# Kernel optimization log

Measured on AMD Instinct MI355X. Metric: run time of the kernel, lower is better.

The kernel has to match this reference:

```python
import jax, jax.numpy as jnp
import numpy as np

B, N, OBS, ACT, H = 262144, 3, 30, 5, 64
IN = OBS + ACT  # 35
NEG_SLOPE_ATT = 0.2   # PyG GATConv default
NEG_SLOPE_MLP = 0.01
LN_EPS = 1e-5


def setup_inputs() -> dict:
    key = jax.random.key(0)
    ks = jax.random.split(key, 24)
    p = lambda k, shape, s=0.1: jax.random.normal(k, shape, jnp.float32) * s
    return {
        "obs": jax.random.normal(ks[0], (B, N * OBS), jnp.float32),
        "action": jax.random.normal(ks[1], (B, N * ACT), jnp.float32),
        "adj_matrix": jax.random.randint(ks[2], (B, N, N), 0, 2, jnp.int32),
        # GAT layer 1 (in=35 -> out=64, 1 head)
        "W1": p(ks[3], (IN, H)), "a1s": p(ks[4], (H,)), "a1d": p(ks[5], (H,)), "b1": jnp.zeros((H,), jnp.float32),
        # GAT layer 2 (in=64 -> out=64, 1 head)
        "W2": p(ks[6], (H, H)), "a2s": p(ks[7], (H,)), "a2d": p(ks[8], (H,)), "b2": jnp.zeros((H,), jnp.float32),
        # output_net: Linear(192,256)+LN, Linear(256,128)+LN, Linear(128,1)
        "Wo1": p(ks[9], (N * H, 256)), "bo1": jnp.zeros((256,), jnp.float32),
        "g1": jnp.ones((256,), jnp.float32), "be1": jnp.zeros((256,), jnp.float32),
        "Wo2": p(ks[10], (256, 128)), "bo2": jnp.zeros((128,), jnp.float32),
        "g2": jnp.ones((128,), jnp.float32), "be2": jnp.zeros((128,), jnp.float32),
        "Wo3": p(ks[11], (128, 1)), "bo3": jnp.zeros((1,), jnp.float32),
    }


def _gat(x, W, a_s, a_d, b, count):
    # x: [B,N,Din], count[b,i,j] = multiplicity of edge j->i (adj^T + self loop)
    z = jnp.einsum('bnd,de->bne', x, W)                      # [B,N,H]
    s_src = jnp.einsum('bnd,d->bn', z, a_s)                  # score contrib of source j
    s_dst = jnp.einsum('bnd,d->bn', z, a_d)                  # score contrib of target i
    e = jax.nn.leaky_relu(s_src[:, None, :] + s_dst[:, :, None], NEG_SLOPE_ATT)  # e[b,i,j]
    cnt = count.astype(z.dtype)
    m = jnp.max(jnp.where(count > 0, e, -jnp.inf), axis=-1, keepdims=True)  # self-loop guarantees finite
    p = cnt * jnp.exp(e - m)                                 # multiplicity-weighted softmax numerator
    alpha = p / jnp.sum(p, axis=-1, keepdims=True)           # [B,N,N]
    return jnp.einsum('bij,bjd->bid', alpha, z) + b


def _ln(x, g, be):
    mu = jnp.mean(x, axis=-1, keepdims=True)
    v = jnp.mean(jnp.square(x - mu), axis=-1, keepdims=True)
    return (x - mu) * jax.lax.rsqrt(v + LN_EPS) * g + be


def reference(obs, action, adj_matrix, W1, a1s, a1d, b1, W2, a2s, a2d, b2,
              Wo1, bo1, g1, be1, Wo2, bo2, g2, be2, Wo3, bo3):
    Bsz = obs.shape[0]
    x = jnp.concatenate([obs.reshape(Bsz, N, OBS), action.reshape(Bsz, N, ACT)], axis=-1)  # [B,N,35]
    # edge multiplicity: adj[b,s,t] means edge s->t; plus one self-loop per node
    count = jnp.swapaxes(adj_matrix, 1, 2) + jnp.eye(N, dtype=adj_matrix.dtype)  # count[b,i,j]
    h = jax.nn.elu(_gat(x, W1, a1s, a1d, b1, count))
    h = _gat(h, W2, a2s, a2d, b2, count)
    h = h.reshape(Bsz, N * H)
    h = jax.nn.leaky_relu(_ln(h @ Wo1 + bo1, g1, be1), NEG_SLOPE_MLP)
    h = jax.nn.leaky_relu(_ln(h @ Wo2 + bo2, g2, be2), NEG_SLOPE_MLP)
    return h @ Wo3 + bo3  # [B,1]
```

## Files before the change

kernel.cpp:

```cpp
#include <hip/hip_runtime.h>
#include <hip/hip_bf16.h>
#include <stdint.h>

#define B_TOT 262144

typedef __attribute__((ext_vector_type(8))) short bf8;
typedef __attribute__((ext_vector_type(16))) float f32x16;

__device__ __forceinline__ uint32_t f2bf(float x) {
  uint32_t u = __float_as_uint(x);
  return (u + 0x7fffu + ((u >> 16) & 1u)) >> 16;
}
__device__ __forceinline__ uint32_t pkbf(float lo, float hi) {
  union { __hip_bfloat162 b; uint32_t u; } c;
  c.b = __float22bfloat162_rn(make_float2(lo, hi));
  return c.u;
}
__device__ __forceinline__ bf8 mkfrag(uint32_t w0, uint32_t w1, uint32_t w2, uint32_t w3) {
  union { uint32_t u[4]; bf8 v; } c;
  c.u[0] = w0; c.u[1] = w1; c.u[2] = w2; c.u[3] = w3;
  return c.v;
}
__device__ __forceinline__ bf8 u4bf8(uint4 v) {
  union { uint4 u; bf8 b; } c; c.u = v; return c.b;
}
__device__ __forceinline__ int swz(int c, int q) { return c * 16 + (q ^ (c & 15)); }

__global__ __launch_bounds__(256) void prep_kernel(
    const int* __restrict__ adj,
    const float* __restrict__ W1, const float* __restrict__ a1s, const float* __restrict__ a1d,
    const float* __restrict__ W2, const float* __restrict__ a2s, const float* __restrict__ a2d,
    const float* __restrict__ Wo1, const float* __restrict__ Wo2,
    uint32_t* __restrict__ cntp, uint16_t* __restrict__ W1F, uint16_t* __restrict__ W2F,
    uint16_t* __restrict__ Wo1F, uint16_t* __restrict__ Wo2F, float* __restrict__ wvec)
{
  const int gid = blockIdx.x * 256 + threadIdx.x;
  if (gid < B_TOT) {
    uint32_t cpv = 0;
    const int* ap = adj + (size_t)gid * 9;
    #pragma unroll
    for (int i = 0; i < 3; ++i)
      #pragma unroll
      for (int j = 0; j < 3; ++j) {
        uint32_t c = (uint32_t)ap[j * 3 + i] + (i == j ? 1u : 0u);
        cpv |= c << (2 * (3 * i + j));
      }
    cntp[gid] = cpv;
  }
  const int e = gid & 7, li = (gid >> 3) & 63;
  const int kfrag = 8 * (e >> 2) + 4 * (li >> 5) + (e & 3);
  if (gid < 3072) {
    const int f = gid >> 9, t = f & 1, ks = f >> 1;
    const int k = ks * 16 + kfrag, row = t * 32 + (li & 31);
    W1F[gid] = (uint16_t)f2bf(k < 35 ? W1[k * 64 + row] : 0.f);
  }
  if (gid < 4096) {
    const int f = gid >> 9, t = f & 1, ks = f >> 1;
    const int k = ks * 16 + kfrag, row = t * 32 + (li & 31);
    W2F[gid] = (uint16_t)f2bf(W2[k * 64 + row]);
  }
  if (gid < 49152) {
    const int rr = gid >> 9, t = rr & 7, ks = rr >> 3;
    const int k = ks * 16 + kfrag, col = t * 32 + (li & 31);
    Wo1F[gid] = (uint16_t)f2bf(Wo1[k * 256 + col]);
  }
  if (gid < 32768) {
    const int rr = gid >> 9, t = rr & 3, ks = rr >> 2;
    const int k = ks * 16 + kfrag, col = t * 32 + (li & 31);
    Wo2F[gid] = (uint16_t)f2bf(Wo2[k * 128 + col]);
  }
  if (gid < 224) {
    if (gid < 48) {
      float s = 0.f; if (gid < 35) for (int d = 0; d < 64; ++d) s += W1[gid * 64 + d] * a1s[d];
      wvec[gid] = s;
    } else if (gid < 96) {
      const int k = gid - 48; float s = 0.f;
      if (k < 35) for (int d = 0; d < 64; ++d) s += W1[k * 64 + d] * a1d[d];
      wvec[64 + k] = s;
    } else if (gid < 160) {
      const int k = gid - 96; float s = 0.f;
      for (int d = 0; d < 64; ++d) s += W2[k * 64 + d] * a2s[d];
      wvec[128 + k] = s;
    } else {
      const int k = gid - 160; float s = 0.f;
      for (int d = 0; d < 64; ++d) s += W2[k * 64 + d] * a2d[d];
      wvec[192 + k] = s;
    }
  }
}

__device__ __forceinline__ void att_alpha(const float (&ss)[3], const float (&sd)[3],
                                          uint32_t cp, float (&al)[3][3])
{
  #pragma unroll
  for (int i = 0; i < 3; ++i) {
    float ev[3]; float mx = -1e30f;
    #pragma unroll
    for (int j = 0; j < 3; ++j) {
      float s = ss[j] + sd[i];
      s = fmaxf(s, 0.2f * s);
      ev[j] = s;
      int c = (cp >> (2 * (3 * i + j))) & 3;
      mx = fmaxf(mx, c ? s : -1e30f);
    }
    float sum = 0.f;
    #pragma unroll
    for (int j = 0; j < 3; ++j) {
      int c = (cp >> (2 * (3 * i + j))) & 3;
      float p = (float)c * __expf(ev[j] - mx);
      al[i][j] = p; sum += p;
    }
    float inv = 1.0f / sum;
    #pragma unroll
    for (int j = 0; j < 3; ++j) al[i][j] *= inv;
  }
}

__device__ __forceinline__ void attention1(const f32x16 (&az)[3][2],
    const float (&ss)[3], const float (&sd)[3], uint32_t cp, int hi,
    const float* __restrict__ bvec, const float* __restrict__ nxs, const float* __restrict__ nxd,
    uint32_t (&Ph)[3][16], float (&ss2)[3], float (&sd2)[3])
{
  float al[3][3];
  att_alpha(ss, sd, cp, al);
  #pragma unroll
  for (int t = 0; t < 2; ++t) {
    float bv[16], nsv[16], ndv[16];
    #pragma unroll
    for (int rq = 0; rq < 4; ++rq) {
      float4 b4 = *reinterpret_cast<const float4*>(bvec + t * 32 + rq * 8 + hi * 4);
      float4 s4 = *reinterpret_cast<const float4*>(nxs + t * 32 + rq * 8 + hi * 4);
      float4 d4 = *reinterpret_cast<const float4*>(nxd + t * 32 + rq * 8 + hi * 4);
      bv[4 * rq + 0] = b4.x; bv[4 * rq + 1] = b4.y; bv[4 * rq + 2] = b4.z; bv[4 * rq + 3] = b4.w;
      nsv[4 * rq + 0] = s4.x; nsv[4 * rq + 1] = s4.y; nsv[4 * rq + 2] = s4.z; nsv[4 * rq + 3] = s4.w;
      ndv[4 * rq + 0] = d4.x; ndv[4 * rq + 1] = d4.y; ndv[4 * rq + 2] = d4.z; ndv[4 * rq + 3] = d4.w;
    }
    #pragma unroll
    for (int i = 0; i < 3; ++i) {
      float hv[16];
      #pragma unroll
      for (int r = 0; r < 16; ++r) {
        float v = bv[r];
        v = fmaf(al[i][0], az[0][t][r], v);
        v = fmaf(al[i][1], az[1][t][r], v);
        v = fmaf(al[i][2], az[2][t][r], v);
        v = v > 0.f ? v : (__expf(v) - 1.f);
        ss2[i] = fmaf(v, nsv[r], ss2[i]); sd2[i] = fmaf(v, ndv[r], sd2[i]);
        hv[r] = v;
      }
      #pragma unroll
      for (int p = 0; p < 8; ++p) Ph[i][t * 8 + p] = pkbf(hv[2 * p], hv[2 * p + 1]);
    }
  }
}

__device__ __forceinline__ void attention2(const f32x16 (&az)[3][2],
    const float (&ss)[3], const float (&sd)[3], uint32_t cp, int hi,
    const float* __restrict__ bvec, uint4* __restrict__ b4p, int c_own)
{
  float al[3][3];
  att_alpha(ss, sd, cp, al);
  #pragma unroll
  for (int t = 0; t < 2; ++t) {
    float bv[16];
    #pragma unroll
    for (int rq = 0; rq < 4; ++rq) {
      float4 b4 = *reinterpret_cast<const float4*>(bvec + t * 32 + rq * 8 + hi * 4);
      bv[4 * rq + 0] = b4.x; bv[4 * rq + 1] = b4.y; bv[4 * rq + 2] = b4.z; bv[4 * rq + 3] = b4.w;
    }
    #pragma unroll
    for (int i = 0; i < 3; ++i) {
      float hv[16];
      #pragma unroll
      for (int r = 0; r < 16; ++r) {
        float v = bv[r];
        v = fmaf(al[i][0], az[0][t][r], v);
        v = fmaf(al[i][1], az[1][t][r], v);
        v = fmaf(al[i][2], az[2][t][r], v);
        hv[r] = v;
      }
      uint32_t w0 = pkbf(hv[0], hv[1]),  w1 = pkbf(hv[2], hv[3]);
      uint32_t w2 = pkbf(hv[4], hv[5]),  w3 = pkbf(hv[6], hv[7]);
      uint32_t w4 = pkbf(hv[8], hv[9]),  w5 = pkbf(hv[10], hv[11]);
      uint32_t w6 = pkbf(hv[12], hv[13]), w7 = pkbf(hv[14], hv[15]);
      b4p[swz(c_own, i * 4 + t * 2 + 0)] = make_uint4(w0, w1, w2, w3);
      b4p[swz(c_own, i * 4 + t * 2 + 1)] = make_uint4(w4, w5, w6, w7);
    }
  }
}

__global__ __launch_bounds__(256, 2) void fused_kernel(
    const float* __restrict__ obs, const float* __restrict__ act,
    const uint32_t* __restrict__ cntp,
    const uint16_t* __restrict__ W1F, const uint16_t* __restrict__ W2F,
    const float* __restrict__ b1, const float* __restrict__ b2,
    const uint16_t* __restrict__ Wo1F, const float* __restrict__ bo1,
    const float* __restrict__ g1, const float* __restrict__ be1,
    const uint16_t* __restrict__ Wo2F, const float* __restrict__ bo2,
    const float* __restrict__ g2, const float* __restrict__ be2,
    const float* __restrict__ Wo3, const float* __restrict__ bo3,
    const float* __restrict__ wvec, float* __restrict__ out)
{
  __shared__ __align__(16) uint32_t buf[16384];
  __shared__ float part[1536];
  uint4* b4p = (uint4*)buf;
  const uint4* b4c = (const uint4*)buf;
  const int tid = threadIdx.x;
  const int l = tid & 63, hi = l >> 5, col = l & 31;
  const int w = tid >> 6;
  const int eb = w * 32 + col;
  const int e = blockIdx.x * 128 + eb;
  const uint32_t cp = cntp[e];
  const float* obs_e = obs + (size_t)e * 90;
  const float* act_e = act + (size_t)e * 15;
  const int h4 = hi * 4;

  bf8 xf[3][3];
  float ss1[3], sd1[3];
  #pragma unroll
  for (int n = 0; n < 3; ++n) {
    const float* on = obs_e + n * 30;
    const float* an = act_e + n * 5;
    const float a0 = an[0], a1 = an[1], a2 = an[2], a3 = an[3], a4 = an[4];
    float2 r00 = *reinterpret_cast<const float2*>(on + h4);
    float2 r01 = *reinterpret_cast<const float2*>(on + h4 + 2);
    float2 r10 = *reinterpret_cast<const float2*>(on + h4 + 8);
    float2 r11 = *reinterpret_cast<const float2*>(on + h4 + 10);
    float2 r20 = *reinterpret_cast<const float2*>(on + h4 + 16);
    float2 r21 = *reinterpret_cast<const float2*>(on + h4 + 18);
    float2 r30 = *reinterpret_cast<const float2*>(on + h4 + 24);
    float2 r31 = *reinterpret_cast<const float2*>(hi ? (on + 24) : (on + 26));
    const float k6 = hi ? a0 : r31.x;
    const float k7 = hi ? a1 : r31.y;
    const float s0 = hi ? 0.f : a2;
    const float s1 = hi ? 0.f : a3;
    const float s2 = hi ? 0.f : a4;
    float ss, sd;
    {
      float4 wS = *reinterpret_cast<const float4*>(wvec + h4);
      float4 wD = *reinterpret_cast<const float4*>(wvec + 64 + h4);
      ss = r00.x * wS.x + r00.y * wS.y; ss = fmaf(r01.x, wS.z, ss); ss = fmaf(r01.y, wS.w, ss);
      sd = r00.x * wD.x + r00.y * wD.y; sd = fmaf(r01.x, wD.z, sd); sd = fmaf(r01.y, wD.w, sd);
      wS = *reinterpret_cast<const float4*>(wvec + h4 + 8);
      wD = *reinterpret_cast<const float4*>(wvec + 64 + h4 + 8);
      ss = fmaf(r10.x, wS.x, ss); ss = fmaf(r10.y, wS.y, ss); ss = fmaf(r11.x, wS.z, ss); ss = fmaf(r11.y, wS.w, ss);
      sd = fmaf(r10.x, wD.x, sd); sd = fmaf(r10.y, wD.y, sd); sd = fmaf(r11.x, wD.z, sd); sd = fmaf(r11.y, wD.w, sd);
      wS = *reinterpret_cast<const float4*>(wvec + h4 + 16);
      wD = *reinterpret_cast<const float4*>(wvec + 64 + h4 + 16);
      ss = fmaf(r20.x, wS.x, ss); ss = fmaf(r20.y, wS.y, ss); ss = fmaf(r21.x, wS.z, ss); ss = fmaf(r21.y, wS.w, ss);
      sd = fmaf(r20.x, wD.x, sd); sd = fmaf(r20.y, wD.y, sd); sd = fmaf(r21.x, wD.z, sd); sd = fmaf(r21.y, wD.w, sd);
      wS = *reinterpret_cast<const float4*>(wvec + h4 + 24);
      wD = *reinterpret_cast<const float4*>(wvec + 64 + h4 + 24);
      ss = fmaf(r30.x, wS.x, ss); ss = fmaf(r30.y, wS.y, ss); ss = fmaf(k6, wS.z, ss); ss = fmaf(k7, wS.w, ss);
      sd = fmaf(r30.x, wD.x, sd); sd = fmaf(r30.y, wD.y, sd); sd = fmaf(k6, wD.z, sd); sd = fmaf(k7, wD.w, sd);
      wS = *reinterpret_cast<const float4*>(wvec + h4 + 32);
      wD = *reinterpret_cast<const float4*>(wvec + 64 + h4 + 32);
      ss = fmaf(s0, wS.x, ss); ss = fmaf(s1, wS.y, ss); ss = fmaf(s2, wS.z, ss);
      sd = fmaf(s0, wD.x, sd); sd = fmaf(s1, wD.y, sd); sd = fmaf(s2, wD.z, sd);
    }
    ss1[n] = ss; sd1[n] = sd;
    xf[0][n] = mkfrag(pkbf(r00.x, r00.y), pkbf(r01.x, r01.y), pkbf(r10.x, r10.y), pkbf(r11.x, r11.y));
    xf[1][n] = mkfrag(pkbf(r20.x, r20.y), pkbf(r21.x, r21.y), pkbf(r30.x, r30.y), pkbf(k6, k7));
    xf[2][n] = mkfrag(pkbf(s0, s1), pkbf(s2, 0.f), 0u, 0u);
  }
  f32x16 az[3][2];
  #pragma unroll
  for (int n = 0; n < 3; ++n)
    #pragma unroll
    for (int t = 0; t < 2; ++t)
      #pragma unroll
      for (int r = 0; r < 16; ++r) az[n][t][r] = 0.f;
  #pragma unroll
  for (int ks = 0; ks < 3; ++ks)
    #pragma unroll
    for (int t = 0; t < 2; ++t) {
      bf8 a = *reinterpret_cast<const bf8*>(W1F + (size_t)(ks * 2 + t) * 512 + l * 8);
      #pragma unroll
      for (int n = 0; n < 3; ++n)
        az[n][t] = __builtin_amdgcn_mfma_f32_32x32x16_bf16(a, xf[ks][n], az[n][t], 0, 0, 0);
    }
  #pragma unroll
  for (int n = 0; n < 3; ++n) {
    ss1[n] += __shfl_xor(ss1[n], 32);
    sd1[n] += __shfl_xor(sd1[n], 32);
  }

  uint32_t Ph1[3][16];
  float ss2[3] = {0, 0, 0}, sd2[3] = {0, 0, 0};
  attention1(az, ss1, sd1, cp, hi, b1, wvec + 128, wvec + 192, Ph1, ss2, sd2);
  #pragma unroll
  for (int n = 0; n < 3; ++n) {
    ss2[n] += __shfl_xor(ss2[n], 32);
    sd2[n] += __shfl_xor(sd2[n], 32);
  }

  f32x16 a2[3][2];
  #pragma unroll
  for (int n = 0; n < 3; ++n)
    #pragma unroll
    for (int t = 0; t < 2; ++t)
      #pragma unroll
      for (int r = 0; r < 16; ++r) a2[n][t][r] = 0.f;
  #pragma unroll
  for (int ks = 0; ks < 4; ++ks) {
    #pragma unroll
    for (int t = 0; t < 2; ++t) {
      bf8 a = *reinterpret_cast<const bf8*>(W2F + (size_t)(ks * 2 + t) * 512 + l * 8);
      #pragma unroll
      for (int n = 0; n < 3; ++n) {
        bf8 br_ = mkfrag(Ph1[n][4 * ks], Ph1[n][4 * ks + 1], Ph1[n][4 * ks + 2], Ph1[n][4 * ks + 3]);
        a2[n][t] = __builtin_amdgcn_mfma_f32_32x32x16_bf16(a, br_, a2[n][t], 0, 0, 0);
      }
    }
  }

  attention2(a2, ss2, sd2, cp, hi, b2, b4p, hi * 128 + eb);
  __syncthreads();

  const int fb1 = w * 64;
  f32x16 acc[2][4];
  #pragma unroll
  for (int t = 0; t < 2; ++t)
    #pragma unroll
    for (int rq = 0; rq < 4; ++rq) {
      float4 b4 = *reinterpret_cast<const float4*>(bo1 + fb1 + t * 32 + rq * 8 + hi * 4);
      #pragma unroll
      for (int eg = 0; eg < 4; ++eg) {
        acc[t][eg][4 * rq + 0] = b4.x; acc[t][eg][4 * rq + 1] = b4.y;
        acc[t][eg][4 * rq + 2] = b4.z; acc[t][eg][4 * rq + 3] = b4.w;
      }
    }
  #pragma unroll
  for (int ks = 0; ks < 12; ++ks) {
    bf8 bfr[4];
    #pragma unroll
    for (int eg = 0; eg < 4; ++eg)
      bfr[eg] = u4bf8(b4c[swz(hi * 128 + eg * 32 + col, ks)]);
    #pragma unroll
    for (int t = 0; t < 2; ++t) {
      bf8 a = *reinterpret_cast<const bf8*>(Wo1F + (size_t)(ks * 8 + w * 2 + t) * 512 + l * 8);
      #pragma unroll
      for (int eg = 0; eg < 4; ++eg)
        acc[t][eg] = __builtin_amdgcn_mfma_f32_32x32x16_bf16(a, bfr[eg], acc[t][eg], 0, 0, 0);
    }
  }
  {
    float psm[4], psq[4];
    #pragma unroll
    for (int eg = 0; eg < 4; ++eg) { psm[eg] = 0.f; psq[eg] = 0.f; }
    #pragma unroll
    for (int t = 0; t < 2; ++t)
      #pragma unroll
      for (int eg = 0; eg < 4; ++eg)
        #pragma unroll
        for (int r = 0; r < 16; ++r) {
          const float v = acc[t][eg][r]; psm[eg] += v; psq[eg] = fmaf(v, v, psq[eg]);
        }
    #pragma unroll
    for (int eg = 0; eg < 4; ++eg) {
      psm[eg] += __shfl_xor(psm[eg], 32);
      psq[eg] += __shfl_xor(psq[eg], 32);
      if (hi == 0) {
        part[w * 128 + eg * 32 + col] = psm[eg];
        part[512 + w * 128 + eg * 32 + col] = psq[eg];
      }
    }
  }
  __syncthreads();
  float mu1[4], rr1[4];
  #pragma unroll
  for (int eg = 0; eg < 4; ++eg) {
    const int ei = eg * 32 + col;
    float s = part[ei] + part[128 + ei] + part[256 + ei] + part[384 + ei];
    float q = part[512 + ei] + part[640 + ei] + part[768 + ei] + part[896 + ei];
    mu1[eg] = s * (1.f / 256.f);
    rr1[eg] = rsqrtf(q * (1.f / 256.f) - mu1[eg] * mu1[eg] + 1e-5f);
  }
  #pragma unroll
  for (int t = 0; t < 2; ++t) {
    float gv[16], bv[16];
    #pragma unroll
    for (int rq = 0; rq < 4; ++rq) {
      float4 gg = *reinterpret_cast<const float4*>(g1 + fb1 + t * 32 + rq * 8 + hi * 4);
      float4 bb = *reinterpret_cast<const float4*>(be1 + fb1 + t * 32 + rq * 8 + hi * 4);
      gv[4 * rq + 0] = gg.x; gv[4 * rq + 1] = gg.y; gv[4 * rq + 2] = gg.z; gv[4 * rq + 3] = gg.w;
      bv[4 * rq + 0] = bb.x; bv[4 * rq + 1] = bb.y; bv[4 * rq + 2] = bb.z; bv[4 * rq + 3] = bb.w;
    }
    #pragma unroll
    for (int eg = 0; eg < 4; ++eg) {
      uint32_t wd[8];
      #pragma unroll
      for (int p = 0; p < 8; ++p) {
        float va = (acc[t][eg][2 * p]     - mu1[eg]) * rr1[eg] * gv[2 * p]     + bv[2 * p];
        float vb = (acc[t][eg][2 * p + 1] - mu1[eg]) * rr1[eg] * gv[2 * p + 1] + bv[2 * p + 1];
        va = fmaxf(va, 0.01f * va);
        vb = fmaxf(vb, 0.01f * vb);
        wd[p] = pkbf(va, vb);
      }
      const int c = hi * 128 + eg * 32 + col;
      b4p[swz(c, w * 4 + t * 2 + 0)] = make_uint4(wd[0], wd[1], wd[2], wd[3]);
      b4p[swz(c, w * 4 + t * 2 + 1)] = make_uint4(wd[4], wd[5], wd[6], wd[7]);
    }
  }
  __syncthreads();

  const int fb2 = w * 32;
  f32x16 acc2[4];
  #pragma unroll
  for (int rq = 0; rq < 4; ++rq) {
    float4 b4 = *reinterpret_cast<const float4*>(bo2 + fb2 + rq * 8 + hi * 4);
    #pragma unroll
    for (int eg = 0; eg < 4; ++eg) {
      acc2[eg][4 * rq + 0] = b4.x; acc2[eg][4 * rq + 1] = b4.y;
      acc2[eg][4 * rq + 2] = b4.z; acc2[eg][4 * rq + 3] = b4.w;
    }
  }
  #pragma unroll
  for (int ks = 0; ks < 16; ++ks) {
    bf8 bfr[4];
    #pragma unroll
    for (int eg = 0; eg < 4; ++eg)
      bfr[eg] = u4bf8(b4c[swz(hi * 128 + eg * 32 + col, ks)]);
    bf8 a = *reinterpret_cast<const bf8*>(Wo2F + (size_t)(ks * 4 + w) * 512 + l * 8);
    #pragma unroll
    for (int eg = 0; eg < 4; ++eg)
      acc2[eg] = __builtin_amdgcn_mfma_f32_32x32x16_bf16(a, bfr[eg], acc2[eg], 0, 0, 0);
  }
  {
    float psm[4], psq[4];
    #pragma unroll
    for (int eg = 0; eg < 4; ++eg) { psm[eg] = 0.f; psq[eg] = 0.f; }
    #pragma unroll
    for (int eg = 0; eg < 4; ++eg)
      #pragma unroll
      for (int r = 0; r < 16; ++r) {
        const float v = acc2[eg][r]; psm[eg] += v; psq[eg] = fmaf(v, v, psq[eg]);
      }
    #pragma unroll
    for (int eg = 0; eg < 4; ++eg) {
      psm[eg] += __shfl_xor(psm[eg], 32);
      psq[eg] += __shfl_xor(psq[eg], 32);
      if (hi == 0) {
        part[w * 128 + eg * 32 + col] = psm[eg];
        part[512 + w * 128 + eg * 32 + col] = psq[eg];
      }
    }
  }
  __syncthreads();
  {
    float dot[4];
    #pragma unroll
    for (int eg = 0; eg < 4; ++eg) {
      const int ei = eg * 32 + col;
      float s = part[ei] + part[128 + ei] + part[256 + ei] + part[384 + ei];
      float q = part[512 + ei] + part[640 + ei] + part[768 + ei] + part[896 + ei];
      const float mu = s * (1.f / 128.f);
      const float rr = rsqrtf(q * (1.f / 128.f) - mu * mu + 1e-5f);
      float d = 0.f;
      #pragma unroll
      for (int rq = 0; rq < 4; ++rq) {
        float4 gg = *reinterpret_cast<const float4*>(g2 + fb2 + rq * 8 + hi * 4);
        float4 bb = *reinterpret_cast<const float4*>(be2 + fb2 + rq * 8 + hi * 4);
        float4 ww = *reinterpret_cast<const float4*>(Wo3 + fb2 + rq * 8 + hi * 4);
        float v;
        v = (acc2[eg][4 * rq + 0] - mu) * rr * gg.x + bb.x; d = fmaf(fmaxf(v, 0.01f * v), ww.x, d);
        v = (acc2[eg][4 * rq + 1] - mu) * rr * gg.y + bb.y; d = fmaf(fmaxf(v, 0.01f * v), ww.y, d);
        v = (acc2[eg][4 * rq + 2] - mu) * rr * gg.z + bb.z; d = fmaf(fmaxf(v, 0.01f * v), ww.z, d);
        v = (acc2[eg][4 * rq + 3] - mu) * rr * gg.w + bb.w; d = fmaf(fmaxf(v, 0.01f * v), ww.w, d);
      }
      dot[eg] = d;
    }
    #pragma unroll
    for (int eg = 0; eg < 4; ++eg) {
      dot[eg] += __shfl_xor(dot[eg], 32);
      if (hi == 0) part[1024 + w * 128 + eg * 32 + col] = dot[eg];
    }
  }
  __syncthreads();
  if (tid < 128) {
    out[blockIdx.x * 128 + tid] = part[1024 + tid] + part[1152 + tid] +
                                  part[1280 + tid] + part[1408 + tid] + bo3[0];
  }
}

extern "C" void kernel_launch(void* const* d_in, const int* in_sizes, int n_in,
                              void* d_out, int out_size, void* d_ws, size_t ws_size,
                              hipStream_t stream) {
  const float* obs  = (const float*)d_in[0];
  const float* actn = (const float*)d_in[1];
  const int*   adj  = (const int*)d_in[2];
  const float* W1   = (const float*)d_in[3];
  const float* a1s  = (const float*)d_in[4];
  const float* a1d  = (const float*)d_in[5];
  const float* b1   = (const float*)d_in[6];
  const float* W2   = (const float*)d_in[7];
  const float* a2s  = (const float*)d_in[8];
  const float* a2d  = (const float*)d_in[9];
  const float* b2   = (const float*)d_in[10];
  const float* Wo1  = (const float*)d_in[11];
  const float* bo1  = (const float*)d_in[12];
  const float* g1   = (const float*)d_in[13];
  const float* be1  = (const float*)d_in[14];
  const float* Wo2  = (const float*)d_in[15];
  const float* bo2  = (const float*)d_in[16];
  const float* g2   = (const float*)d_in[17];
  const float* be2  = (const float*)d_in[18];
  const float* Wo3  = (const float*)d_in[19];
  const float* bo3  = (const float*)d_in[20];

  char* ws = (char*)d_ws;
  uint32_t* cntp = (uint32_t*)ws;
  uint16_t* W1F  = (uint16_t*)(ws + 1048576);
  uint16_t* W2F  = (uint16_t*)(ws + 1048576 + 8192);
  uint16_t* Wo1F = (uint16_t*)(ws + 1048576 + 16384);
  uint16_t* Wo2F = (uint16_t*)(ws + 1048576 + 114688);
  float*    wvec = (float*)(ws + 1048576 + 180224);
  float* outp = (float*)d_out;

  prep_kernel<<<1024, 256, 0, stream>>>(adj, W1, a1s, a1d, W2, a2s, a2d, Wo1, Wo2,
                                        cntp, W1F, W2F, Wo1F, Wo2F, wvec);
  fused_kernel<<<2048, 256, 0, stream>>>(obs, actn, cntp, W1F, W2F, b1, b2,
                                         Wo1F, bo1, g1, be1, Wo2F, bo2, g2, be2,
                                         Wo3, bo3, wvec, outp);
}
```

Baseline: 111.8 us.

## Switch fused kernel to 16x16x32 MFMA tiles with 64-sample blocks

```diff
diff --git a/kernel.cpp b/kernel.cpp
--- a/kernel.cpp
+++ b/kernel.cpp
@@ -5,7 +5,7 @@
 #define B_TOT 262144
 
 typedef __attribute__((ext_vector_type(8))) short bf8;
-typedef __attribute__((ext_vector_type(16))) float f32x16;
+typedef __attribute__((ext_vector_type(4))) float f32x4;
 
 __device__ __forceinline__ uint32_t f2bf(float x) {
   uint32_t u = __float_as_uint(x);
@@ -21,10 +21,6 @@
   c.u[0] = w0; c.u[1] = w1; c.u[2] = w2; c.u[3] = w3;
   return c.v;
 }
-__device__ __forceinline__ bf8 u4bf8(uint4 v) {
-  union { uint4 u; bf8 b; } c; c.u = v; return c.b;
-}
-__device__ __forceinline__ int swz(int c, int q) { return c * 16 + (q ^ (c & 15)); }
 
 __global__ __launch_bounds__(256) void prep_kernel(
     const int* __restrict__ adj,
@@ -48,25 +44,26 @@
     cntp[gid] = cpv;
   }
   const int e = gid & 7, li = (gid >> 3) & 63;
-  const int kfrag = 8 * (e >> 2) + 4 * (li >> 5) + (e & 3);
-  if (gid < 3072) {
-    const int f = gid >> 9, t = f & 1, ks = f >> 1;
-    const int k = ks * 16 + kfrag, row = t * 32 + (li & 31);
+  const int kf = (e & 3) + 4 * ((li >> 4) & 3) + 16 * (e >> 2);
+  const int sp = li & 15;
+  if (gid < 4096) {
+    const int f = gid >> 9, t = f & 3, ks = f >> 2;
+    const int k = ks * 32 + kf, row = t * 16 + sp;
     W1F[gid] = (uint16_t)f2bf(k < 35 ? W1[k * 64 + row] : 0.f);
   }
   if (gid < 4096) {
-    const int f = gid >> 9, t = f & 1, ks = f >> 1;
-    const int k = ks * 16 + kfrag, row = t * 32 + (li & 31);
+    const int f = gid >> 9, t = f & 3, ks = f >> 2;
+    const int k = ks * 32 + kf, row = t * 16 + sp;
     W2F[gid] = (uint16_t)f2bf(W2[k * 64 + row]);
   }
   if (gid < 49152) {
-    const int rr = gid >> 9, t = rr & 7, ks = rr >> 3;
-    const int k = ks * 16 + kfrag, col = t * 32 + (li & 31);
+    const int f = gid >> 9, t = f & 15, ks = f >> 4;
+    const int k = ks * 32 + kf, col = t * 16 + sp;
     Wo1F[gid] = (uint16_t)f2bf(Wo1[k * 256 + col]);
   }
   if (gid < 32768) {
-    const int rr = gid >> 9, t = rr & 3, ks = rr >> 2;
-    const int k = ks * 16 + kfrag, col = t * 32 + (li & 31);
+    const int f = gid >> 9, t = f & 7, ks = f >> 3;
+    const int k = ks * 32 + kf, col = t * 16 + sp;
     Wo2F[gid] = (uint16_t)f2bf(Wo2[k * 128 + col]);
   }
   if (gid < 224) {
@@ -116,80 +113,7 @@
   }
 }
 
-__device__ __forceinline__ void attention1(const f32x16 (&az)[3][2],
-    const float (&ss)[3], const float (&sd)[3], uint32_t cp, int hi,
-    const float* __restrict__ bvec, const float* __restrict__ nxs, const float* __restrict__ nxd,
-    uint32_t (&Ph)[3][16], float (&ss2)[3], float (&sd2)[3])
-{
-  float al[3][3];
-  att_alpha(ss, sd, cp, al);
-  #pragma unroll
-  for (int t = 0; t < 2; ++t) {
-    float bv[16], nsv[16], ndv[16];
-    #pragma unroll
-    for (int rq = 0; rq < 4; ++rq) {
-      float4 b4 = *reinterpret_cast<const float4*>(bvec + t * 32 + rq * 8 + hi * 4);
-      float4 s4 = *reinterpret_cast<const float4*>(nxs + t * 32 + rq * 8 + hi * 4);
-      float4 d4 = *reinterpret_cast<const float4*>(nxd + t * 32 + rq * 8 + hi * 4);
-      bv[4 * rq + 0] = b4.x; bv[4 * rq + 1] = b4.y; bv[4 * rq + 2] = b4.z; bv[4 * rq + 3] = b4.w;
-      nsv[4 * rq + 0] = s4.x; nsv[4 * rq + 1] = s4.y; nsv[4 * rq + 2] = s4.z; nsv[4 * rq + 3] = s4.w;
-      ndv[4 * rq + 0] = d4.x; ndv[4 * rq + 1] = d4.y; ndv[4 * rq + 2] = d4.z; ndv[4 * rq + 3] = d4.w;
-    }
-    #pragma unroll
-    for (int i = 0; i < 3; ++i) {
-      float hv[16];
-      #pragma unroll
-      for (int r = 0; r < 16; ++r) {
-        float v = bv[r];
-        v = fmaf(al[i][0], az[0][t][r], v);
-        v = fmaf(al[i][1], az[1][t][r], v);
-        v = fmaf(al[i][2], az[2][t][r], v);
-        v = v > 0.f ? v : (__expf(v) - 1.f);
-        ss2[i] = fmaf(v, nsv[r], ss2[i]); sd2[i] = fmaf(v, ndv[r], sd2[i]);
-        hv[r] = v;
-      }
-      #pragma unroll
-      for (int p = 0; p < 8; ++p) Ph[i][t * 8 + p] = pkbf(hv[2 * p], hv[2 * p + 1]);
-    }
-  }
-}
-
-__device__ __forceinline__ void attention2(const f32x16 (&az)[3][2],
-    const float (&ss)[3], const float (&sd)[3], uint32_t cp, int hi,
-    const float* __restrict__ bvec, uint4* __restrict__ b4p, int c_own)
-{
-  float al[3][3];
-  att_alpha(ss, sd, cp, al);
-  #pragma unroll
-  for (int t = 0; t < 2; ++t) {
-    float bv[16];
-    #pragma unroll
-    for (int rq = 0; rq < 4; ++rq) {
-      float4 b4 = *reinterpret_cast<const float4*>(bvec + t * 32 + rq * 8 + hi * 4);
-      bv[4 * rq + 0] = b4.x; bv[4 * rq + 1] = b4.y; bv[4 * rq + 2] = b4.z; bv[4 * rq + 3] = b4.w;
-    }
-    #pragma unroll
-    for (int i = 0; i < 3; ++i) {
-      float hv[16];
-      #pragma unroll
-      for (int r = 0; r < 16; ++r) {
-        float v = bv[r];
-        v = fmaf(al[i][0], az[0][t][r], v);
-        v = fmaf(al[i][1], az[1][t][r], v);
-        v = fmaf(al[i][2], az[2][t][r], v);
-        hv[r] = v;
-      }
-      uint32_t w0 = pkbf(hv[0], hv[1]),  w1 = pkbf(hv[2], hv[3]);
-      uint32_t w2 = pkbf(hv[4], hv[5]),  w3 = pkbf(hv[6], hv[7]);
-      uint32_t w4 = pkbf(hv[8], hv[9]),  w5 = pkbf(hv[10], hv[11]);
-      uint32_t w6 = pkbf(hv[12], hv[13]), w7 = pkbf(hv[14], hv[15]);
-      b4p[swz(c_own, i * 4 + t * 2 + 0)] = make_uint4(w0, w1, w2, w3);
-      b4p[swz(c_own, i * 4 + t * 2 + 1)] = make_uint4(w4, w5, w6, w7);
-    }
-  }
-}
-
-__global__ __launch_bounds__(256, 2) void fused_kernel(
+__global__ __launch_bounds__(256, 4) void fused_kernel(
     const float* __restrict__ obs, const float* __restrict__ act,
     const uint32_t* __restrict__ cntp,
     const uint16_t* __restrict__ W1F, const uint16_t* __restrict__ W2F,
@@ -201,168 +125,205 @@
     const float* __restrict__ Wo3, const float* __restrict__ bo3,
     const float* __restrict__ wvec, float* __restrict__ out)
 {
-  __shared__ __align__(16) uint32_t buf[16384];
-  __shared__ float part[1536];
-  uint4* b4p = (uint4*)buf;
-  const uint4* b4c = (const uint4*)buf;
+  __shared__ __align__(16) uint32_t buf[8320];
+  __shared__ float part[1024];
   const int tid = threadIdx.x;
-  const int l = tid & 63, hi = l >> 5, col = l & 31;
+  const int l = tid & 63, g = l >> 4, cl = l & 15;
   const int w = tid >> 6;
-  const int eb = w * 32 + col;
-  const int e = blockIdx.x * 128 + eb;
+  const int g4 = g * 4;
+  const int eb = w * 16 + cl;
+  const int e = blockIdx.x * 64 + eb;
   const uint32_t cp = cntp[e];
   const float* obs_e = obs + (size_t)e * 90;
   const float* act_e = act + (size_t)e * 15;
-  const int h4 = hi * 4;
-
-  bf8 xf[3][3];
+
+  bf8 xf0[3], xf1[3];
   float ss1[3], sd1[3];
   #pragma unroll
   for (int n = 0; n < 3; ++n) {
     const float* on = obs_e + n * 30;
     const float* an = act_e + n * 5;
     const float a0 = an[0], a1 = an[1], a2 = an[2], a3 = an[3], a4 = an[4];
-    float2 r00 = *reinterpret_cast<const float2*>(on + h4);
-    float2 r01 = *reinterpret_cast<const float2*>(on + h4 + 2);
-    float2 r10 = *reinterpret_cast<const float2*>(on + h4 + 8);
-    float2 r11 = *reinterpret_cast<const float2*>(on + h4 + 10);
-    float2 r20 = *reinterpret_cast<const float2*>(on + h4 + 16);
-    float2 r21 = *reinterpret_cast<const float2*>(on + h4 + 18);
-    float2 r30 = *reinterpret_cast<const float2*>(on + h4 + 24);
-    float2 r31 = *reinterpret_cast<const float2*>(hi ? (on + 24) : (on + 26));
-    const float k6 = hi ? a0 : r31.x;
-    const float k7 = hi ? a1 : r31.y;
-    const float s0 = hi ? 0.f : a2;
-    const float s1 = hi ? 0.f : a3;
-    const float s2 = hi ? 0.f : a4;
+    float2 r00 = *reinterpret_cast<const float2*>(on + g4);
+    float2 r01 = *reinterpret_cast<const float2*>(on + g4 + 2);
+    float2 r10 = *reinterpret_cast<const float2*>(on + 16 + g4);
+    float2 r11 = *reinterpret_cast<const float2*>(on + (g == 3 ? 24 : 18 + g4));
+    const float k6 = (g == 3) ? a0 : r11.x;
+    const float k7 = (g == 3) ? a1 : r11.y;
+    const float s0 = (g == 0) ? a2 : 0.f;
+    const float s1 = (g == 0) ? a3 : 0.f;
+    const float s2 = (g == 0) ? a4 : 0.f;
     float ss, sd;
     {
-      float4 wS = *reinterpret_cast<const float4*>(wvec + h4);
-      float4 wD = *reinterpret_cast<const float4*>(wvec + 64 + h4);
+      float4 wS = *reinterpret_cast<const float4*>(wvec + g4);
+      float4 wD = *reinterpret_cast<const float4*>(wvec + 64 + g4);
       ss = r00.x * wS.x + r00.y * wS.y; ss = fmaf(r01.x, wS.z, ss); ss = fmaf(r01.y, wS.w, ss);
       sd = r00.x * wD.x + r00.y * wD.y; sd = fmaf(r01.x, wD.z, sd); sd = fmaf(r01.y, wD.w, sd);
-      wS = *reinterpret_cast<const float4*>(wvec + h4 + 8);
-      wD = *reinterpret_cast<const float4*>(wvec + 64 + h4 + 8);
-      ss = fmaf(r10.x, wS.x, ss); ss = fmaf(r10.y, wS.y, ss); ss = fmaf(r11.x, wS.z, ss); ss = fmaf(r11.y, wS.w, ss);
-      sd = fmaf(r10.x, wD.x, sd); sd = fmaf(r10.y, wD.y, sd); sd = fmaf(r11.x, wD.z, sd); sd = fmaf(r11.y, wD.w, sd);
-      wS = *reinterpret_cast<const float4*>(wvec + h4 + 16);
-      wD = *reinterpret_cast<const float4*>(wvec + 64 + h4 + 16);
-      ss = fmaf(r20.x, wS.x, ss); ss = fmaf(r20.y, wS.y, ss); ss = fmaf(r21.x, wS.z, ss); ss = fmaf(r21.y, wS.w, ss);
-      sd = fmaf(r20.x, wD.x, sd); sd = fmaf(r20.y, wD.y, sd); sd = fmaf(r21.x, wD.z, sd); sd = fmaf(r21.y, wD.w, sd);
-      wS = *reinterpret_cast<const float4*>(wvec + h4 + 24);
-      wD = *reinterpret_cast<const float4*>(wvec + 64 + h4 + 24);
-      ss = fmaf(r30.x, wS.x, ss); ss = fmaf(r30.y, wS.y, ss); ss = fmaf(k6, wS.z, ss); ss = fmaf(k7, wS.w, ss);
-      sd = fmaf(r30.x, wD.x, sd); sd = fmaf(r30.y, wD.y, sd); sd = fmaf(k6, wD.z, sd); sd = fmaf(k7, wD.w, sd);
-      wS = *reinterpret_cast<const float4*>(wvec + h4 + 32);
-      wD = *reinterpret_cast<const float4*>(wvec + 64 + h4 + 32);
+      wS = *reinterpret_cast<const float4*>(wvec + 16 + g4);
+      wD = *reinterpret_cast<const float4*>(wvec + 80 + g4);
+      ss = fmaf(r10.x, wS.x, ss); ss = fmaf(r10.y, wS.y, ss); ss = fmaf(k6, wS.z, ss); ss = fmaf(k7, wS.w, ss);
+      sd = fmaf(r10.x, wD.x, sd); sd = fmaf(r10.y, wD.y, sd); sd = fmaf(k6, wD.z, sd); sd = fmaf(k7, wD.w, sd);
+      wS = *reinterpret_cast<const float4*>(wvec + 32 + g4);
+      wD = *reinterpret_cast<const float4*>(wvec + 96 + g4);
       ss = fmaf(s0, wS.x, ss); ss = fmaf(s1, wS.y, ss); ss = fmaf(s2, wS.z, ss);
       sd = fmaf(s0, wD.x, sd); sd = fmaf(s1, wD.y, sd); sd = fmaf(s2, wD.z, sd);
     }
     ss1[n] = ss; sd1[n] = sd;
-    xf[0][n] = mkfrag(pkbf(r00.x, r00.y), pkbf(r01.x, r01.y), pkbf(r10.x, r10.y), pkbf(r11.x, r11.y));
-    xf[1][n] = mkfrag(pkbf(r20.x, r20.y), pkbf(r21.x, r21.y), pkbf(r30.x, r30.y), pkbf(k6, k7));
-    xf[2][n] = mkfrag(pkbf(s0, s1), pkbf(s2, 0.f), 0u, 0u);
-  }
-  f32x16 az[3][2];
+    xf0[n] = mkfrag(pkbf(r00.x, r00.y), pkbf(r01.x, r01.y), pkbf(r10.x, r10.y), pkbf(k6, k7));
+    xf1[n] = mkfrag(pkbf(s0, s1), pkbf(s2, 0.f), 0u, 0u);
+  }
+  f32x4 az[3][4];
   #pragma unroll
   for (int n = 0; n < 3; ++n)
     #pragma unroll
-    for (int t = 0; t < 2; ++t)
-      #pragma unroll
-      for (int r = 0; r < 16; ++r) az[n][t][r] = 0.f;
-  #pragma unroll
-  for (int ks = 0; ks < 3; ++ks)
-    #pragma unroll
-    for (int t = 0; t < 2; ++t) {
-      bf8 a = *reinterpret_cast<const bf8*>(W1F + (size_t)(ks * 2 + t) * 512 + l * 8);
+    for (int t = 0; t < 4; ++t)
+      #pragma unroll
+      for (int r = 0; r < 4; ++r) az[n][t][r] = 0.f;
+  #pragma unroll
+  for (int ks = 0; ks < 2; ++ks)
+    #pragma unroll
+    for (int t = 0; t < 4; ++t) {
+      bf8 a = *reinterpret_cast<const bf8*>(W1F + (size_t)((ks * 4 + t) * 64 + l) * 8);
       #pragma unroll
       for (int n = 0; n < 3; ++n)
-        az[n][t] = __builtin_amdgcn_mfma_f32_32x32x16_bf16(a, xf[ks][n], az[n][t], 0, 0, 0);
+        az[n][t] = __builtin_amdgcn_mfma_f32_16x16x32_bf16(a, ks ? xf1[n] : xf0[n], az[n][t], 0, 0, 0);
     }
   #pragma unroll
   for (int n = 0; n < 3; ++n) {
-    ss1[n] += __shfl_xor(ss1[n], 32);
-    sd1[n] += __shfl_xor(sd1[n], 32);
-  }
-
-  uint32_t Ph1[3][16];
+    ss1[n] += __shfl_xor(ss1[n], 16); ss1[n] += __shfl_xor(ss1[n], 32);
+    sd1[n] += __shfl_xor(sd1[n], 16); sd1[n] += __shfl_xor(sd1[n], 32);
+  }
+
+  uint32_t Ph[3][4][2];
   float ss2[3] = {0, 0, 0}, sd2[3] = {0, 0, 0};
-  attention1(az, ss1, sd1, cp, hi, b1, wvec + 128, wvec + 192, Ph1, ss2, sd2);
-  #pragma unroll
-  for (int n = 0; n < 3; ++n) {
-    ss2[n] += __shfl_xor(ss2[n], 32);
-    sd2[n] += __shfl_xor(sd2[n], 32);
-  }
-
-  f32x16 a2[3][2];
+  {
+    float al[3][3];
+    att_alpha(ss1, sd1, cp, al);
+    #pragma unroll
+    for (int t = 0; t < 4; ++t) {
+      float4 b4 = *reinterpret_cast<const float4*>(b1 + t * 16 + g4);
+      float4 s4 = *reinterpret_cast<const float4*>(wvec + 128 + t * 16 + g4);
+      float4 d4 = *reinterpret_cast<const float4*>(wvec + 192 + t * 16 + g4);
+      const float bv[4] = {b4.x, b4.y, b4.z, b4.w};
+      const float sv[4] = {s4.x, s4.y, s4.z, s4.w};
+      const float dv[4] = {d4.x, d4.y, d4.z, d4.w};
+      #pragma unroll
+      for (int i = 0; i < 3; ++i) {
+        float hv[4];
+        #pragma unroll
+        for (int r = 0; r < 4; ++r) {
+          float v = bv[r];
+          v = fmaf(al[i][0], az[0][t][r], v);
+          v = fmaf(al[i][1], az[1][t][r], v);
+          v = fmaf(al[i][2], az[2][t][r], v);
+          v = v > 0.f ? v : (__expf(v) - 1.f);
+          ss2[i] = fmaf(v, sv[r], ss2[i]);
+          sd2[i] = fmaf(v, dv[r], sd2[i]);
+          hv[r] = v;
+        }
+        Ph[i][t][0] = pkbf(hv[0], hv[1]);
+        Ph[i][t][1] = pkbf(hv[2], hv[3]);
+      }
+    }
+  }
+  #pragma unroll
+  for (int i = 0; i < 3; ++i) {
+    ss2[i] += __shfl_xor(ss2[i], 16); ss2[i] += __shfl_xor(ss2[i], 32);
+    sd2[i] += __shfl_xor(sd2[i], 16); sd2[i] += __shfl_xor(sd2[i], 32);
+  }
+
+  f32x4 a2z[3][4];
   #pragma unroll
   for (int n = 0; n < 3; ++n)
     #pragma unroll
-    for (int t = 0; t < 2; ++t)
-      #pragma unroll
-      for (int r = 0; r < 16; ++r) a2[n][t][r] = 0.f;
-  #pragma unroll
-  for (int ks = 0; ks < 4; ++ks) {
-    #pragma unroll
-    for (int t = 0; t < 2; ++t) {
-      bf8 a = *reinterpret_cast<const bf8*>(W2F + (size_t)(ks * 2 + t) * 512 + l * 8);
-      #pragma unroll
-      for (int n = 0; n < 3; ++n) {
-        bf8 br_ = mkfrag(Ph1[n][4 * ks], Ph1[n][4 * ks + 1], Ph1[n][4 * ks + 2], Ph1[n][4 * ks + 3]);
-        a2[n][t] = __builtin_amdgcn_mfma_f32_32x32x16_bf16(a, br_, a2[n][t], 0, 0, 0);
-      }
-    }
-  }
-
-  attention2(a2, ss2, sd2, cp, hi, b2, b4p, hi * 128 + eb);
+    for (int t = 0; t < 4; ++t)
+      #pragma unroll
+      for (int r = 0; r < 4; ++r) a2z[n][t][r] = 0.f;
+  #pragma unroll
+  for (int ks = 0; ks < 2; ++ks) {
+    bf8 br[3];
+    #pragma unroll
+    for (int n = 0; n < 3; ++n)
+      br[n] = mkfrag(Ph[n][2 * ks][0], Ph[n][2 * ks][1], Ph[n][2 * ks + 1][0], Ph[n][2 * ks + 1][1]);
+    #pragma unroll
+    for (int t = 0; t < 4; ++t) {
+      bf8 aW = *reinterpret_cast<const bf8*>(W2F + (size_t)((ks * 4 + t) * 64 + l) * 8);
+      #pragma unroll
+      for (int n = 0; n < 3; ++n)
+        a2z[n][t] = __builtin_amdgcn_mfma_f32_16x16x32_bf16(aW, br[n], a2z[n][t], 0, 0, 0);
+    }
+  }
+
+  {
+    float al[3][3];
+    att_alpha(ss2, sd2, cp, al);
+    #pragma unroll
+    for (int t = 0; t < 4; ++t) {
+      float4 b4 = *reinterpret_cast<const float4*>(b2 + t * 16 + g4);
+      const float bv[4] = {b4.x, b4.y, b4.z, b4.w};
+      #pragma unroll
+      for (int i = 0; i < 3; ++i) {
+        float hv[4];
+        #pragma unroll
+        for (int r = 0; r < 4; ++r) {
+          float v = bv[r];
+          v = fmaf(al[i][0], a2z[0][t][r], v);
+          v = fmaf(al[i][1], a2z[1][t][r], v);
+          v = fmaf(al[i][2], a2z[2][t][r], v);
+          hv[r] = v;
+        }
+        *reinterpret_cast<uint2*>(buf + eb * 98 + i * 32 + t * 8 + 2 * g) =
+            make_uint2(pkbf(hv[0], hv[1]), pkbf(hv[2], hv[3]));
+      }
+    }
+  }
   __syncthreads();
 
-  const int fb1 = w * 64;
-  f32x16 acc[2][4];
-  #pragma unroll
-  for (int t = 0; t < 2; ++t)
-    #pragma unroll
-    for (int rq = 0; rq < 4; ++rq) {
-      float4 b4 = *reinterpret_cast<const float4*>(bo1 + fb1 + t * 32 + rq * 8 + hi * 4);
-      #pragma unroll
-      for (int eg = 0; eg < 4; ++eg) {
-        acc[t][eg][4 * rq + 0] = b4.x; acc[t][eg][4 * rq + 1] = b4.y;
-        acc[t][eg][4 * rq + 2] = b4.z; acc[t][eg][4 * rq + 3] = b4.w;
-      }
-    }
-  #pragma unroll
-  for (int ks = 0; ks < 12; ++ks) {
+  const int ft0 = w * 4;
+  f32x4 acc[4][4];
+  #pragma unroll
+  for (int t = 0; t < 4; ++t) {
+    float4 b4 = *reinterpret_cast<const float4*>(bo1 + (ft0 + t) * 16 + g4);
+    #pragma unroll
+    for (int eg = 0; eg < 4; ++eg) {
+      acc[t][eg][0] = b4.x; acc[t][eg][1] = b4.y; acc[t][eg][2] = b4.z; acc[t][eg][3] = b4.w;
+    }
+  }
+  #pragma unroll
+  for (int ks = 0; ks < 6; ++ks) {
     bf8 bfr[4];
     #pragma unroll
-    for (int eg = 0; eg < 4; ++eg)
-      bfr[eg] = u4bf8(b4c[swz(hi * 128 + eg * 32 + col, ks)]);
-    #pragma unroll
-    for (int t = 0; t < 2; ++t) {
-      bf8 a = *reinterpret_cast<const bf8*>(Wo1F + (size_t)(ks * 8 + w * 2 + t) * 512 + l * 8);
+    for (int eg = 0; eg < 4; ++eg) {
+      const uint32_t* p0 = buf + (eg * 16 + cl) * 98 + ks * 16 + 2 * g;
+      uint2 u0 = *reinterpret_cast<const uint2*>(p0);
+      uint2 u1 = *reinterpret_cast<const uint2*>(p0 + 8);
+      bfr[eg] = mkfrag(u0.x, u0.y, u1.x, u1.y);
+    }
+    #pragma unroll
+    for (int t = 0; t < 4; ++t) {
+      bf8 a = *reinterpret_cast<const bf8*>(Wo1F + (size_t)((ks * 16 + ft0 + t) * 64 + l) * 8);
       #pragma unroll
       for (int eg = 0; eg < 4; ++eg)
-        acc[t][eg] = __builtin_amdgcn_mfma_f32_32x32x16_bf16(a, bfr[eg], acc[t][eg], 0, 0, 0);
+        acc[t][eg] = __builtin_amdgcn_mfma_f32_16x16x32_bf16(a, bfr[eg], acc[t][eg], 0, 0, 0);
     }
   }
   {
-    float psm[4], psq[4];
-    #pragma unroll
-    for (int eg = 0; eg < 4; ++eg) { psm[eg] = 0.f; psq[eg] = 0.f; }
-    #pragma unroll
-    for (int t = 0; t < 2; ++t)
+    float psm[4] = {0, 0, 0, 0}, psq[4] = {0, 0, 0, 0};
+    #pragma unroll
+    for (int t = 0; t < 4; ++t)
       #pragma unroll
       for (int eg = 0; eg < 4; ++eg)
         #pragma unroll
-        for (int r = 0; r < 16; ++r) {
+        for (int r = 0; r < 4; ++r) {
           const float v = acc[t][eg][r]; psm[eg] += v; psq[eg] = fmaf(v, v, psq[eg]);
         }
     #pragma unroll
     for (int eg = 0; eg < 4; ++eg) {
-      psm[eg] += __shfl_xor(psm[eg], 32);
-      psq[eg] += __shfl_xor(psq[eg], 32);
-      if (hi == 0) {
-        part[w * 128 + eg * 32 + col] = psm[eg];
-        part[512 + w * 128 + eg * 32 + col] = psq[eg];
+      psm[eg] += __shfl_xor(psm[eg], 16); psm[eg] += __shfl_xor(psm[eg], 32);
+      psq[eg] += __shfl_xor(psq[eg], 16); psq[eg] += __shfl_xor(psq[eg], 32);
+      if (g == 0) {
+        part[w * 64 + eg * 16 + cl] = psm[eg];
+        part[256 + w * 64 + eg * 16 + cl] = psq[eg];
       }
     }
   }
@@ -370,79 +331,77 @@
   float mu1[4], rr1[4];
   #pragma unroll
   for (int eg = 0; eg < 4; ++eg) {
-    const int ei = eg * 32 + col;
-    float s = part[ei] + part[128 + ei] + part[256 + ei] + part[384 + ei];
-    float q = part[512 + ei] + part[640 + ei] + part[768 + ei] + part[896 + ei];
+    const int ei = eg * 16 + cl;
+    float s = part[ei] + part[64 + ei] + part[128 + ei] + part[192 + ei];
+    float q = part[256 + ei] + part[320 + ei] + part[384 + ei] + part[448 + ei];
     mu1[eg] = s * (1.f / 256.f);
     rr1[eg] = rsqrtf(q * (1.f / 256.f) - mu1[eg] * mu1[eg] + 1e-5f);
   }
   #pragma unroll
+  for (int t = 0; t < 4; ++t) {
+    float4 gg = *reinterpret_cast<const float4*>(g1 + (ft0 + t) * 16 + g4);
+    float4 bb = *reinterpret_cast<const float4*>(be1 + (ft0 + t) * 16 + g4);
+    const float gv[4] = {gg.x, gg.y, gg.z, gg.w};
+    const float bv[4] = {bb.x, bb.y, bb.z, bb.w};
+    #pragma unroll
+    for (int eg = 0; eg < 4; ++eg) {
+      float vv[4];
+      #pragma unroll
+      for (int r = 0; r < 4; ++r) {
+        float v = (acc[t][eg][r] - mu1[eg]) * rr1[eg] * gv[r] + bv[r];
+        vv[r] = fmaxf(v, 0.01f * v);
+      }
+      *reinterpret_cast<uint2*>(buf + (eg * 16 + cl) * 130 + (ft0 + t) * 8 + 2 * g) =
+          make_uint2(pkbf(vv[0], vv[1]), pkbf(vv[2], vv[3]));
+    }
+  }
+  __syncthreads();
+
+  const int ft2 = w * 2;
+  f32x4 acc2[2][4];
+  #pragma unroll
   for (int t = 0; t < 2; ++t) {
-    float gv[16], bv[16];
-    #pragma unroll
-    for (int rq = 0; rq < 4; ++rq) {
-      float4 gg = *reinterpret_cast<const float4*>(g1 + fb1 + t * 32 + rq * 8 + hi * 4);
-      float4 bb = *reinterpret_cast<const float4*>(be1 + fb1 + t * 32 + rq * 8 + hi * 4);
-      gv[4 * rq + 0] = gg.x; gv[4 * rq + 1] = gg.y; gv[4 * rq + 2] = gg.z; gv[4 * rq + 3] = gg.w;
-      bv[4 * rq + 0] = bb.x; bv[4 * rq + 1] = bb.y; bv[4 * rq + 2] = bb.z; bv[4 * rq + 3] = bb.w;
-    }
-    #pragma unroll
-    for (int eg = 0; eg < 4; ++eg) {
-      uint32_t wd[8];
-      #pragma unroll
-      for (int p = 0; p < 8; ++p) {
-        float va = (acc[t][eg][2 * p]     - mu1[eg]) * rr1[eg] * gv[2 * p]     + bv[2 * p];
-        float vb = (acc[t][eg][2 * p + 1] - mu1[eg]) * rr1[eg] * gv[2 * p + 1] + bv[2 * p + 1];
-        va = fmaxf(va, 0.01f * va);
-        vb = fmaxf(vb, 0.01f * vb);
-        wd[p] = pkbf(va, vb);
-      }
-      const int c = hi * 128 + eg * 32 + col;
-      b4p[swz(c, w * 4 + t * 2 + 0)] = make_uint4(wd[0], wd[1], wd[2], wd[3]);
-      b4p[swz(c, w * 4 + t * 2 + 1)] = make_uint4(wd[4], wd[5], wd[6], wd[7]);
-    }
-  }
-  __syncthreads();
-
-  const int fb2 = w * 32;
-  f32x16 acc2[4];
-  #pragma unroll
-  for (int rq = 0; rq < 4; ++rq) {
-    float4 b4 = *reinterpret_cast<const float4*>(bo2 + fb2 + rq * 8 + hi * 4);
-    #pragma unroll
-    for (int eg = 0; eg < 4; ++eg) {
-      acc2[eg][4 * rq + 0] = b4.x; acc2[eg][4 * rq + 1] = b4.y;
-      acc2[eg][4 * rq + 2] = b4.z; acc2[eg][4 * rq + 3] = b4.w;
-    }
-  }
-  #pragma unroll
-  for (int ks = 0; ks < 16; ++ks) {
+    float4 b4 = *reinterpret_cast<const float4*>(bo2 + (ft2 + t) * 16 + g4);
+    #pragma unroll
+    for (int eg = 0; eg < 4; ++eg) {
+      acc2[t][eg][0] = b4.x; acc2[t][eg][1] = b4.y; acc2[t][eg][2] = b4.z; acc2[t][eg][3] = b4.w;
+    }
+  }
+  #pragma unroll
+  for (int ks = 0; ks < 8; ++ks) {
     bf8 bfr[4];
     #pragma unroll
-    for (int eg = 0; eg < 4; ++eg)
-      bfr[eg] = u4bf8(b4c[swz(hi * 128 + eg * 32 + col, ks)]);
-    bf8 a = *reinterpret_cast<const bf8*>(Wo2F + (size_t)(ks * 4 + w) * 512 + l * 8);
-    #pragma unroll
-    for (int eg = 0; eg < 4; ++eg)
-      acc2[eg] = __builtin_amdgcn_mfma_f32_32x32x16_bf16(a, bfr[eg], acc2[eg], 0, 0, 0);
+    for (int eg = 0; eg < 4; ++eg) {
+      const uint32_t* p0 = buf + (eg * 16 + cl) * 130 + ks * 16 + 2 * g;
+      uint2 u0 = *reinterpret_cast<const uint2*>(p0);
+      uint2 u1 = *reinterpret_cast<const uint2*>(p0 + 8);
+      bfr[eg] = mkfrag(u0.x, u0.y, u1.x, u1.y);
+    }
+    #pragma unroll
+    for (int t = 0; t < 2; ++t) {
+      bf8 a = *reinterpret_cast<const bf8*>(Wo2F + (size_t)((ks * 8 + ft2 + t) * 64 + l) * 8);
+      #pragma unroll
+      for (int eg = 0; eg < 4; ++eg)
+        acc2[t][eg] = __builtin_amdgcn_mfma_f32_16x16x32_bf16(a, bfr[eg], acc2[t][eg], 0, 0, 0);
+    }
   }
   {
-    float psm[4], psq[4];
-    #pragma unroll
-    for (int eg = 0; eg < 4; ++eg) { psm[eg] = 0.f; psq[eg] = 0.f; }
-    #pragma unroll
-    for (int eg = 0; eg < 4; ++eg)
-      #pragma unroll
-      for (int r = 0; r < 16; ++r) {
-        const float v = acc2[eg][r]; psm[eg] += v; psq[eg] = fmaf(v, v, psq[eg]);
-      }
-    #pragma unroll
-    for (int eg = 0; eg < 4; ++eg) {
-      psm[eg] += __shfl_xor(psm[eg], 32);
-      psq[eg] += __shfl_xor(psq[eg], 32);
-      if (hi == 0) {
-        part[w * 128 + eg * 32 + col] = psm[eg];
-        part[512 + w * 128 + eg * 32 + col] = psq[eg];
+    float psm[4] = {0, 0, 0, 0}, psq[4] = {0, 0, 0, 0};
+    #pragma unroll
+    for (int t = 0; t < 2; ++t)
+      #pragma unroll
+      for (int eg = 0; eg < 4; ++eg)
+        #pragma unroll
+        for (int r = 0; r < 4; ++r) {
+          const float v = acc2[t][eg][r]; psm[eg] += v; psq[eg] = fmaf(v, v, psq[eg]);
+        }
+    #pragma unroll
+    for (int eg = 0; eg < 4; ++eg) {
+      psm[eg] += __shfl_xor(psm[eg], 16); psm[eg] += __shfl_xor(psm[eg], 32);
+      psq[eg] += __shfl_xor(psq[eg], 16); psq[eg] += __shfl_xor(psq[eg], 32);
+      if (g == 0) {
+        part[w * 64 + eg * 16 + cl] = psm[eg];
+        part[256 + w * 64 + eg * 16 + cl] = psq[eg];
       }
     }
   }
@@ -451,35 +410,38 @@
     float dot[4];
     #pragma unroll
     for (int eg = 0; eg < 4; ++eg) {
-      const int ei = eg * 32 + col;
-      float s = part[ei] + part[128 + ei] + part[256 + ei] + part[384 + ei];
-      float q = part[512 + ei] + part[640 + ei] + part[768 + ei] + part[896 + ei];
+      const int ei = eg * 16 + cl;
+      float s = part[ei] + part[64 + ei] + part[128 + ei] + part[192 + ei];
+      float q = part[256 + ei] + part[320 + ei] + part[384 + ei] + part[448 + ei];
       const float mu = s * (1.f / 128.f);
       const float rr = rsqrtf(q * (1.f / 128.f) - mu * mu + 1e-5f);
       float d = 0.f;
       #pragma unroll
-      for (int rq = 0; rq < 4; ++rq) {
-        float4 gg = *reinterpret_cast<const float4*>(g2 + fb2 + rq * 8 + hi * 4);
-        float4 bb = *reinterpret_cast<const float4*>(be2 + fb2 + rq * 8 + hi * 4);
-        float4 ww = *reinterpret_cast<const float4*>(Wo3 + fb2 + rq * 8 + hi * 4);
-        float v;
-        v = (acc2[eg][4 * rq + 0] - mu) * rr * gg.x + bb.x; d = fmaf(fmaxf(v, 0.01f * v), ww.x, d);
-        v = (acc2[eg][4 * rq + 1] - mu) * rr * gg.y + bb.y; d = fmaf(fmaxf(v, 0.01f * v), ww.y, d);
-        v = (acc2[eg][4 * rq + 2] - mu) * rr * gg.z + bb.z; d = fmaf(fmaxf(v, 0.01f * v), ww.z, d);
-        v = (acc2[eg][4 * rq + 3] - mu) * rr * gg.w + bb.w; d = fmaf(fmaxf(v, 0.01f * v), ww.w, d);
+      for (int t = 0; t < 2; ++t) {
+        float4 gg = *reinterpret_cast<const float4*>(g2 + (ft2 + t) * 16 + g4);
+        float4 bb = *reinterpret_cast<const float4*>(be2 + (ft2 + t) * 16 + g4);
+        float4 ww = *reinterpret_cast<const float4*>(Wo3 + (ft2 + t) * 16 + g4);
+        const float gv[4] = {gg.x, gg.y, gg.z, gg.w};
+        const float bv[4] = {bb.x, bb.y, bb.z, bb.w};
+        const float wv[4] = {ww.x, ww.y, ww.z, ww.w};
+        #pragma unroll
+        for (int r = 0; r < 4; ++r) {
+          float v = (acc2[t][eg][r] - mu) * rr * gv[r] + bv[r];
+          d = fmaf(fmaxf(v, 0.01f * v), wv[r], d);
+        }
       }
       dot[eg] = d;
     }
     #pragma unroll
     for (int eg = 0; eg < 4; ++eg) {
-      dot[eg] += __shfl_xor(dot[eg], 32);
-      if (hi == 0) part[1024 + w * 128 + eg * 32 + col] = dot[eg];
+      dot[eg] += __shfl_xor(dot[eg], 16); dot[eg] += __shfl_xor(dot[eg], 32);
+      if (g == 0) part[512 + w * 64 + eg * 16 + cl] = dot[eg];
     }
   }
   __syncthreads();
-  if (tid < 128) {
-    out[blockIdx.x * 128 + tid] = part[1024 + tid] + part[1152 + tid] +
-                                  part[1280 + tid] + part[1408 + tid] + bo3[0];
+  if (tid < 64) {
+    out[blockIdx.x * 64 + tid] = part[512 + tid] + part[576 + tid] +
+                                 part[640 + tid] + part[704 + tid] + bo3[0];
   }
 }
 
@@ -519,7 +481,7 @@
 
   prep_kernel<<<1024, 256, 0, stream>>>(adj, W1, a1s, a1d, W2, a2s, a2d, Wo1, Wo2,
                                         cntp, W1F, W2F, Wo1F, Wo2F, wvec);
-  fused_kernel<<<2048, 256, 0, stream>>>(obs, actn, cntp, W1F, W2F, b1, b2,
+  fused_kernel<<<4096, 256, 0, stream>>>(obs, actn, cntp, W1F, W2F, b1, b2,
                                          Wo1F, bo1, g1, be1, Wo2F, bo2, g2, be2,
                                          Wo3, bo3, wvec, outp);
 }
```

Result: slower. 271.9 us (+143.2%).
